# Optimization experiments

Hardware: AMD Instinct MI355X
Metric: run time of the kernel (lower is better)

## Reference

```python
import jax, jax.numpy as jnp
import numpy as np
import math

D = 512      # input_size == hidden_size
TAU = 4      # length of att/spatial lists
N = 16384    # tokens (batch*H*W)

def setup_inputs() -> dict:
    key = jax.random.key(0)
    ks = jax.random.split(key, 16)
    s = 1.0 / math.sqrt(D)
    return {
        "T_t": jax.random.normal(ks[0], (N, D), jnp.float32),
        "S_t": jax.random.normal(ks[1], (N, D), jnp.float32),
        "t_att": jax.random.normal(ks[2], (TAU, N, D), jnp.float32),
        "s_att": jax.random.normal(ks[3], (TAU, N, D), jnp.float32),
        "t_spatial": jax.random.normal(ks[4], (TAU, N, D), jnp.float32),
        "s_spatial": jax.random.normal(ks[5], (TAU, N, D), jnp.float32),
        # fl_t: Linear(D, 3D); fl_t_next: Linear(D, D); same for s
        "W_t": jax.random.uniform(ks[6], (3 * D, D), jnp.float32, -s, s),
        "b_t": jax.random.uniform(ks[7], (3 * D,), jnp.float32, -s, s),
        "W_tn": jax.random.uniform(ks[8], (D, D), jnp.float32, -s, s),
        "b_tn": jax.random.uniform(ks[9], (D,), jnp.float32, -s, s),
        "W_s": jax.random.uniform(ks[10], (3 * D, D), jnp.float32, -s, s),
        "b_s": jax.random.uniform(ks[11], (3 * D,), jnp.float32, -s, s),
        "W_sn": jax.random.uniform(ks[12], (D, D), jnp.float32, -s, s),
        "b_sn": jax.random.uniform(ks[13], (D,), jnp.float32, -s, s),
    }

def reference(T_t, S_t, t_att, s_att, t_spatial, s_spatial,
              W_t, b_t, W_tn, b_tn, W_s, b_s, W_sn, b_sn):
    d = T_t.shape[-1]
    scale = 1.0 / jnp.sqrt(jnp.asarray(d, T_t.dtype))
    s_next = S_t @ W_sn.T + b_sn          # [N, D]
    t_next = T_t @ W_tn.T + b_tn          # [N, D]

    # trend weights: dot-product along feature dim, softmax over tau axis
    w_s = jax.nn.softmax(jnp.einsum('knd,nd->kn', s_att, s_next) * scale, axis=0)
    w_t = jax.nn.softmax(jnp.einsum('knd,nd->kn', t_spatial, t_next) * scale, axis=0)
    T_trend = jnp.einsum('knd,kn->nd', t_att, w_s)      # [N, D]
    S_trend = jnp.einsum('knd,kn->nd', s_spatial, w_t)  # [N, D]

    t_gate = jax.nn.sigmoid(t_next)
    s_gate = jax.nn.sigmoid(s_next)
    T_fusion = T_t * t_gate + (1.0 - t_gate) * T_trend
    S_fusion = S_t * s_gate + (1.0 - s_gate) * S_trend

    T_concat = T_fusion @ W_t.T + b_t     # [N, 3D]
    S_concat = S_fusion @ W_s.T + b_s
    t_g, t_t, t_s = jnp.split(T_concat, 3, axis=1)
    s_g, s_t, s_s = jnp.split(S_concat, 3, axis=1)
    T_gate = jax.nn.sigmoid(t_g)
    S_gate = jax.nn.sigmoid(s_g)
    T_new = T_gate * t_t + (1.0 - T_gate) * s_t
    S_new = S_gate * s_s + (1.0 - S_gate) * t_s
    return T_new, S_new
```

## Files before the change

kernel.cpp:

```cpp
#include <hip/hip_runtime.h>

#define NTOK 16384
#define DIM 512
#define NTAU 4

typedef __attribute__((ext_vector_type(4))) float f32x4;
typedef __attribute__((ext_vector_type(8))) short bf16x8;
typedef __attribute__((ext_vector_type(4))) unsigned short u16x4;
typedef __attribute__((ext_vector_type(8))) unsigned short u16x8;

__device__ inline unsigned short f2bf(float f) {
    union { float f; unsigned int u; } v; v.f = f;
    unsigned int u = v.u + 0x7FFFu + ((v.u >> 16) & 1u);
    return (unsigned short)(u >> 16);
}

__device__ inline void bf8_to_f32(u16x8 h, f32x4& a, f32x4& b) {
    union { unsigned int u; float f; } t;
#pragma unroll
    for (int e = 0; e < 4; e++) { t.u = ((unsigned int)h[e]) << 16; a[e] = t.f; }
#pragma unroll
    for (int e = 0; e < 4; e++) { t.u = ((unsigned int)h[4 + e]) << 16; b[e] = t.f; }
}

#define NTLOAD4(p) __builtin_nontemporal_load((const f32x4*)(p))

__global__ void convert_f32_bf16(const float* __restrict__ src,
                                 unsigned short* __restrict__ dst, int n4) {
    int i = blockIdx.x * blockDim.x + threadIdx.x;
    if (i < n4) {
        f32x4 v = ((const f32x4*)src)[i];
        u16x4 o;
        o[0] = f2bf(v[0]); o[1] = f2bf(v[1]); o[2] = f2bf(v[2]); o[3] = f2bf(v[3]);
        ((u16x4*)dst)[i] = o;
    }
}

__global__ __launch_bounds__(256, 2) void gemm_next(
    const float* __restrict__ A, const unsigned short* __restrict__ W,
    const float* __restrict__ bias, unsigned short* __restrict__ out)
{
    __shared__ unsigned short lA[128][40];
    __shared__ unsigned short lB[128][40];
    const int tid = threadIdx.x;
    const int id = blockIdx.x + 4 * blockIdx.y;
    const int xcd = id & 7;
    const int idx = id >> 3;
    const int m0 = (xcd * 16 + (idx >> 2)) * 128;
    const int n0 = (idx & 3) * 128;
    const int lane = tid & 63;
    const int w = tid >> 6;
    const int wr = w >> 1, wc = w & 1;

    f32x4 acc[4][4];
#pragma unroll
    for (int i = 0; i < 4; i++)
#pragma unroll
        for (int j = 0; j < 4; j++) acc[i][j] = (f32x4){0.f, 0.f, 0.f, 0.f};

    const int arow = tid >> 3;
    const int acol = (tid & 7) * 4;
    const int brow = tid >> 2;
    const int bcol = (tid & 3) * 8;

    for (int k0 = 0; k0 < DIM; k0 += 32) {
#pragma unroll
        for (int i = 0; i < 4; i++) {
            int r = arow + 32 * i;
            f32x4 v = *(const f32x4*)(A + (size_t)(m0 + r) * DIM + k0 + acol);
            u16x4 o;
            o[0] = f2bf(v[0]); o[1] = f2bf(v[1]); o[2] = f2bf(v[2]); o[3] = f2bf(v[3]);
            *(u16x4*)&lA[r][acol] = o;
        }
#pragma unroll
        for (int i = 0; i < 2; i++) {
            int r = brow + 64 * i;
            u16x8 v = *(const u16x8*)(W + (size_t)(n0 + r) * DIM + k0 + bcol);
            *(u16x8*)&lB[r][bcol] = v;
        }
        __syncthreads();

        bf16x8 af[4], bfr[4];
#pragma unroll
        for (int i = 0; i < 4; i++)
            af[i] = *(const bf16x8*)&lA[wr * 64 + i * 16 + (lane & 15)][(lane >> 4) * 8];
#pragma unroll
        for (int j = 0; j < 4; j++)
            bfr[j] = *(const bf16x8*)&lB[wc * 64 + j * 16 + (lane & 15)][(lane >> 4) * 8];
#pragma unroll
        for (int i = 0; i < 4; i++)
#pragma unroll
            for (int j = 0; j < 4; j++)
                acc[i][j] = __builtin_amdgcn_mfma_f32_16x16x32_bf16(af[i], bfr[j], acc[i][j], 0, 0, 0);
        __syncthreads();
    }

#pragma unroll
    for (int j = 0; j < 4; j++) {
        int n = n0 + wc * 64 + j * 16 + (lane & 15);
        float bv = bias[n];
#pragma unroll
        for (int i = 0; i < 4; i++) {
            int mbase = m0 + wr * 64 + i * 16 + (lane >> 4) * 4;
#pragma unroll
            for (int r = 0; r < 4; r++)
                out[(size_t)(mbase + r) * DIM + n] = f2bf(acc[i][j][r] + bv);
        }
    }
}

__global__ __launch_bounds__(256) void fuse_stream(
    const float* __restrict__ T_t, const float* __restrict__ S_t,
    const float* __restrict__ t_att, const float* __restrict__ s_att,
    const float* __restrict__ t_spatial, const float* __restrict__ s_spatial,
    const unsigned short* __restrict__ t_next, const unsigned short* __restrict__ s_next,
    unsigned short* __restrict__ Tf, unsigned short* __restrict__ Sf)
{
    const int lane = threadIdx.x & 63;
    const int n = (blockIdx.x << 2) + (threadIdx.x >> 6);
    const int c = lane * 8;
    const size_t rb = (size_t)n * DIM + c;
    const float scale = 0.04419417382415922f;

    f32x4 tn_a, tn_b, sn_a, sn_b;
    bf8_to_f32(*(const u16x8*)(t_next + rb), tn_a, tn_b);
    bf8_to_f32(*(const u16x8*)(s_next + rb), sn_a, sn_b);

    f32x4 p1s[NTAU][2], p1t[NTAU][2];
#pragma unroll
    for (int k = 0; k < NTAU; k++) {
        const size_t kb = ((size_t)k * NTOK + n) * DIM + c;
        p1s[k][0] = NTLOAD4(s_att + kb);
        p1s[k][1] = NTLOAD4(s_att + kb + 4);
        p1t[k][0] = NTLOAD4(t_spatial + kb);
        p1t[k][1] = NTLOAD4(t_spatial + kb + 4);
    }

    float dws[NTAU], dwt[NTAU];
#pragma unroll
    for (int k = 0; k < NTAU; k++) {
        f32x4 a0 = p1s[k][0], a1 = p1s[k][1];
        f32x4 b0 = p1t[k][0], b1 = p1t[k][1];
        dws[k] = a0[0]*sn_a[0]+a0[1]*sn_a[1]+a0[2]*sn_a[2]+a0[3]*sn_a[3]
               + a1[0]*sn_b[0]+a1[1]*sn_b[1]+a1[2]*sn_b[2]+a1[3]*sn_b[3];
        dwt[k] = b0[0]*tn_a[0]+b0[1]*tn_a[1]+b0[2]*tn_a[2]+b0[3]*tn_a[3]
               + b1[0]*tn_b[0]+b1[1]*tn_b[1]+b1[2]*tn_b[2]+b1[3]*tn_b[3];
    }

    f32x4 p2t[NTAU][2], p2s[NTAU][2];
#pragma unroll
    for (int k = 0; k < NTAU; k++) {
        const size_t kb = ((size_t)k * NTOK + n) * DIM + c;
        p2t[k][0] = NTLOAD4(t_att + kb);
        p2t[k][1] = NTLOAD4(t_att + kb + 4);
        p2s[k][0] = NTLOAD4(s_spatial + kb);
        p2s[k][1] = NTLOAD4(s_spatial + kb + 4);
    }
    f32x4 Ta = *(const f32x4*)(T_t + rb);
    f32x4 Tb = *(const f32x4*)(T_t + rb + 4);
    f32x4 Sa = *(const f32x4*)(S_t + rb);
    f32x4 Sb = *(const f32x4*)(S_t + rb + 4);

#pragma unroll
    for (int k = 0; k < NTAU; k++) {
        float v = dws[k];
#pragma unroll
        for (int off = 32; off; off >>= 1) v += __shfl_xor(v, off);
        dws[k] = v * scale;
        float u = dwt[k];
#pragma unroll
        for (int off = 32; off; off >>= 1) u += __shfl_xor(u, off);
        dwt[k] = u * scale;
    }

    float ws_[NTAU], wt_[NTAU];
    {
        float ms = fmaxf(fmaxf(dws[0], dws[1]), fmaxf(dws[2], dws[3]));
        float mt = fmaxf(fmaxf(dwt[0], dwt[1]), fmaxf(dwt[2], dwt[3]));
        float ssum = 0.f, tsum = 0.f;
#pragma unroll
        for (int k = 0; k < NTAU; k++) {
            ws_[k] = __expf(dws[k] - ms); ssum += ws_[k];
            wt_[k] = __expf(dwt[k] - mt); tsum += wt_[k];
        }
        float rs = 1.f / ssum, rt = 1.f / tsum;
#pragma unroll
        for (int k = 0; k < NTAU; k++) { ws_[k] *= rs; wt_[k] *= rt; }
    }

    f32x4 Tta = {0,0,0,0}, Ttb = {0,0,0,0}, Sta = {0,0,0,0}, Stb = {0,0,0,0};
#pragma unroll
    for (int k = 0; k < NTAU; k++) {
        float wk = ws_[k], vk = wt_[k];
#pragma unroll
        for (int e = 0; e < 4; e++) {
            Tta[e] += wk * p2t[k][0][e]; Ttb[e] += wk * p2t[k][1][e];
            Sta[e] += vk * p2s[k][0][e]; Stb[e] += vk * p2s[k][1][e];
        }
    }

    u16x8 oT, oS;
#pragma unroll
    for (int e = 0; e < 4; e++) {
        float gt_a = 1.f / (1.f + __expf(-tn_a[e]));
        float gt_b = 1.f / (1.f + __expf(-tn_b[e]));
        float gs_a = 1.f / (1.f + __expf(-sn_a[e]));
        float gs_b = 1.f / (1.f + __expf(-sn_b[e]));
        oT[e]     = f2bf(Ta[e] * gt_a + (1.f - gt_a) * Tta[e]);
        oT[4 + e] = f2bf(Tb[e] * gt_b + (1.f - gt_b) * Ttb[e]);
        oS[e]     = f2bf(Sa[e] * gs_a + (1.f - gs_a) * Sta[e]);
        oS[4 + e] = f2bf(Sb[e] * gs_b + (1.f - gs_b) * Stb[e]);
    }
    *(u16x8*)(Tf + rb) = oT;
    *(u16x8*)(Sf + rb) = oS;
}

__global__ __launch_bounds__(256, 2) void gemm_final(
    const unsigned short* __restrict__ Tf, const unsigned short* __restrict__ Sf,
    const unsigned short* __restrict__ Wt, const unsigned short* __restrict__ Ws,
    const float* __restrict__ bt, const float* __restrict__ bs,
    float* __restrict__ out)
{
    __shared__ unsigned short lT[128][40];
    __shared__ unsigned short lS[128][40];
    __shared__ unsigned short lW[6][32][40];
    const int tid = threadIdx.x;
    const int id = blockIdx.x + 16 * blockIdx.y;
    const int xcd = id & 7;
    const int idx = id >> 3;
    const int m0 = (xcd * 16 + (idx >> 4)) * 128;
    const int j0 = (idx & 15) * 32;
    const int lane = tid & 63;
    const int w = tid >> 6, wr = w >> 1, wc = w & 1;

    f32x4 acc[6][4];
#pragma unroll
    for (int g = 0; g < 6; g++)
#pragma unroll
        for (int i = 0; i < 4; i++) acc[g][i] = (f32x4){0.f, 0.f, 0.f, 0.f};

    const int arow = tid >> 2;
    const int acol = (tid & 3) * 8;

    for (int k0 = 0; k0 < DIM; k0 += 32) {
#pragma unroll
        for (int i = 0; i < 2; i++) {
            int r = arow + 64 * i;
            *(u16x8*)&lT[r][acol] = *(const u16x8*)(Tf + (size_t)(m0 + r) * DIM + k0 + acol);
            *(u16x8*)&lS[r][acol] = *(const u16x8*)(Sf + (size_t)(m0 + r) * DIM + k0 + acol);
        }
#pragma unroll
        for (int i = 0; i < 3; i++) {
            int cidx = tid + 256 * i;
            int g = cidx >> 7;
            int rr = (cidx >> 2) & 31;
            int ch = (cidx & 3) * 8;
            const unsigned short* src = (g < 3) ? Wt : Ws;
            int row = (g % 3) * DIM + j0 + rr;
            *(u16x8*)&lW[g][rr][ch] = *(const u16x8*)(src + (size_t)row * DIM + k0 + ch);
        }
        __syncthreads();

        bf16x8 aT[4], aS[4];
#pragma unroll
        for (int i = 0; i < 4; i++) {
            aT[i] = *(const bf16x8*)&lT[wr * 64 + i * 16 + (lane & 15)][(lane >> 4) * 8];
            aS[i] = *(const bf16x8*)&lS[wr * 64 + i * 16 + (lane & 15)][(lane >> 4) * 8];
        }
#pragma unroll
        for (int g = 0; g < 6; g++) {
            bf16x8 bw = *(const bf16x8*)&lW[g][wc * 16 + (lane & 15)][(lane >> 4) * 8];
#pragma unroll
            for (int i = 0; i < 4; i++)
                acc[g][i] = __builtin_amdgcn_mfma_f32_16x16x32_bf16(
                    (g < 3) ? aT[i] : aS[i], bw, acc[g][i], 0, 0, 0);
        }
        __syncthreads();
    }

    const int j = j0 + wc * 16 + (lane & 15);
    const float btg = bt[j], btt = bt[512 + j], bts = bt[1024 + j];
    const float bsg = bs[j], bst = bs[512 + j], bss = bs[1024 + j];
#pragma unroll
    for (int i = 0; i < 4; i++) {
        int mbase = m0 + wr * 64 + i * 16 + (lane >> 4) * 4;
#pragma unroll
        for (int r = 0; r < 4; r++) {
            float TG = acc[0][i][r] + btg;
            float TT = acc[1][i][r] + btt;
            float TS = acc[2][i][r] + bts;
            float SG = acc[3][i][r] + bsg;
            float ST = acc[4][i][r] + bst;
            float SS = acc[5][i][r] + bss;
            float gT = 1.f / (1.f + __expf(-TG));
            float gS = 1.f / (1.f + __expf(-SG));
            size_t m = (size_t)(mbase + r);
            out[m * DIM + j] = gT * TT + (1.f - gT) * ST;
            out[(size_t)NTOK * DIM + m * DIM + j] = gS * SS + (1.f - gS) * TS;
        }
    }
}

extern "C" void kernel_launch(void* const* d_in, const int* in_sizes, int n_in,
                              void* d_out, int out_size, void* d_ws, size_t ws_size,
                              hipStream_t stream) {
    const float* T_t       = (const float*)d_in[0];
    const float* S_t       = (const float*)d_in[1];
    const float* t_att     = (const float*)d_in[2];
    const float* s_att     = (const float*)d_in[3];
    const float* t_spatial = (const float*)d_in[4];
    const float* s_spatial = (const float*)d_in[5];
    const float* W_t  = (const float*)d_in[6];
    const float* b_t  = (const float*)d_in[7];
    const float* W_tn = (const float*)d_in[8];
    const float* b_tn = (const float*)d_in[9];
    const float* W_s  = (const float*)d_in[10];
    const float* b_s  = (const float*)d_in[11];
    const float* W_sn = (const float*)d_in[12];
    const float* b_sn = (const float*)d_in[13];
    float* out = (float*)d_out;

    char* ws = (char*)d_ws;
    unsigned short* t_next = (unsigned short*)(ws + 0);
    unsigned short* s_next = (unsigned short*)(ws + 16777216);
    unsigned short* Tf     = (unsigned short*)(ws + 33554432);
    unsigned short* Sf     = (unsigned short*)(ws + 50331648);
    unsigned short* Wtn_b  = (unsigned short*)(ws + 67108864);
    unsigned short* Wsn_b  = (unsigned short*)(ws + 67633152);
    unsigned short* Wt_b   = (unsigned short*)(ws + 68157440);
    unsigned short* Ws_b   = (unsigned short*)(ws + 69730304);

    const int n_sq = 512 * 512 / 4, n_big = 1536 * 512 / 4;
    convert_f32_bf16<<<(n_sq + 255) / 256, 256, 0, stream>>>(W_tn, Wtn_b, n_sq);
    convert_f32_bf16<<<(n_sq + 255) / 256, 256, 0, stream>>>(W_sn, Wsn_b, n_sq);
    convert_f32_bf16<<<(n_big + 255) / 256, 256, 0, stream>>>(W_t, Wt_b, n_big);
    convert_f32_bf16<<<(n_big + 255) / 256, 256, 0, stream>>>(W_s, Ws_b, n_big);

    dim3 g1(DIM / 128, NTOK / 128);
    gemm_next<<<g1, 256, 0, stream>>>(T_t, Wtn_b, b_tn, t_next);
    gemm_next<<<g1, 256, 0, stream>>>(S_t, Wsn_b, b_sn, s_next);

    fuse_stream<<<4096, 256, 0, stream>>>(T_t, S_t, t_att, s_att, t_spatial, s_spatial,
                                          t_next, s_next, Tf, Sf);

    dim3 g3(DIM / 32, NTOK / 128);
    gemm_final<<<g3, 256, 0, stream>>>(Tf, Sf, Wt_b, Ws_b, b_t, b_s, out);
}
```

Baseline: 292.5 us.

## Double-buffer final GEMM with direct LDS loads, merge weight conversions, hoist stream loads

The final GEMM now double-buffers its shared-memory tiles. It fills them with global_load_lds direct-to-LDS copies using an XOR-swizzled layout instead of padded rows, so the next K tile loads while MFMAs run on the current one. The four weight-conversion launches become one kernel. In fuse_stream, all the big tau-stream loads are issued up front before any computation, so more memory traffic is in flight. The cost is higher register pressure in fuse_stream and twice the LDS footprint in the GEMM.

```diff
diff --git a/kernel.cpp b/kernel.cpp
--- a/kernel.cpp
+++ b/kernel.cpp
@@ -8,6 +8,7 @@
 typedef __attribute__((ext_vector_type(8))) short bf16x8;
 typedef __attribute__((ext_vector_type(4))) unsigned short u16x4;
 typedef __attribute__((ext_vector_type(8))) unsigned short u16x8;
+typedef unsigned int u32;
 
 __device__ inline unsigned short f2bf(float f) {
     union { float f; unsigned int u; } v; v.f = f;
@@ -25,15 +26,25 @@
 
 #define NTLOAD4(p) __builtin_nontemporal_load((const f32x4*)(p))
 
-__global__ void convert_f32_bf16(const float* __restrict__ src,
-                                 unsigned short* __restrict__ dst, int n4) {
-    int i = blockIdx.x * blockDim.x + threadIdx.x;
-    if (i < n4) {
-        f32x4 v = ((const f32x4*)src)[i];
-        u16x4 o;
-        o[0] = f2bf(v[0]); o[1] = f2bf(v[1]); o[2] = f2bf(v[2]); o[3] = f2bf(v[3]);
-        ((u16x4*)dst)[i] = o;
-    }
+__device__ __forceinline__ void gload16(const void* g, void* l) {
+    __builtin_amdgcn_global_load_lds((const __attribute__((address_space(1))) u32*)g,
+                                     (__attribute__((address_space(3))) u32*)l, 16, 0, 0);
+}
+
+__global__ void convert_all(const float* __restrict__ a, const float* __restrict__ b,
+                            const float* __restrict__ c, const float* __restrict__ d,
+                            unsigned short* __restrict__ oa, unsigned short* __restrict__ ob,
+                            unsigned short* __restrict__ oc, unsigned short* __restrict__ od) {
+    int i = blockIdx.x * 256 + threadIdx.x;
+    const float* s; unsigned short* t; int off;
+    if (i < 65536)       { s = a; t = oa; off = i; }
+    else if (i < 131072) { s = b; t = ob; off = i - 65536; }
+    else if (i < 327680) { s = c; t = oc; off = i - 131072; }
+    else                 { s = d; t = od; off = i - 327680; }
+    f32x4 v = ((const f32x4*)s)[off];
+    u16x4 o;
+    o[0] = f2bf(v[0]); o[1] = f2bf(v[1]); o[2] = f2bf(v[2]); o[3] = f2bf(v[3]);
+    ((u16x4*)t)[off] = o;
 }
 
 __global__ __launch_bounds__(256, 2) void gemm_next(
@@ -122,11 +133,9 @@
     const size_t rb = (size_t)n * DIM + c;
     const float scale = 0.04419417382415922f;
 
-    f32x4 tn_a, tn_b, sn_a, sn_b;
-    bf8_to_f32(*(const u16x8*)(t_next + rb), tn_a, tn_b);
-    bf8_to_f32(*(const u16x8*)(s_next + rb), sn_a, sn_b);
-
-    f32x4 p1s[NTAU][2], p1t[NTAU][2];
+    u16x8 hn_t = *(const u16x8*)(t_next + rb);
+    u16x8 hn_s = *(const u16x8*)(s_next + rb);
+    f32x4 p1s[NTAU][2], p1t[NTAU][2], p2t[NTAU][2], p2s[NTAU][2];
 #pragma unroll
     for (int k = 0; k < NTAU; k++) {
         const size_t kb = ((size_t)k * NTOK + n) * DIM + c;
@@ -135,6 +144,22 @@
         p1t[k][0] = NTLOAD4(t_spatial + kb);
         p1t[k][1] = NTLOAD4(t_spatial + kb + 4);
     }
+#pragma unroll
+    for (int k = 0; k < NTAU; k++) {
+        const size_t kb = ((size_t)k * NTOK + n) * DIM + c;
+        p2t[k][0] = NTLOAD4(t_att + kb);
+        p2t[k][1] = NTLOAD4(t_att + kb + 4);
+        p2s[k][0] = NTLOAD4(s_spatial + kb);
+        p2s[k][1] = NTLOAD4(s_spatial + kb + 4);
+    }
+    f32x4 Ta = *(const f32x4*)(T_t + rb);
+    f32x4 Tb = *(const f32x4*)(T_t + rb + 4);
+    f32x4 Sa = *(const f32x4*)(S_t + rb);
+    f32x4 Sb = *(const f32x4*)(S_t + rb + 4);
+
+    f32x4 tn_a, tn_b, sn_a, sn_b;
+    bf8_to_f32(hn_t, tn_a, tn_b);
+    bf8_to_f32(hn_s, sn_a, sn_b);
 
     float dws[NTAU], dwt[NTAU];
 #pragma unroll
@@ -146,21 +171,6 @@
         dwt[k] = b0[0]*tn_a[0]+b0[1]*tn_a[1]+b0[2]*tn_a[2]+b0[3]*tn_a[3]
                + b1[0]*tn_b[0]+b1[1]*tn_b[1]+b1[2]*tn_b[2]+b1[3]*tn_b[3];
     }
-
-    f32x4 p2t[NTAU][2], p2s[NTAU][2];
-#pragma unroll
-    for (int k = 0; k < NTAU; k++) {
-        const size_t kb = ((size_t)k * NTOK + n) * DIM + c;
-        p2t[k][0] = NTLOAD4(t_att + kb);
-        p2t[k][1] = NTLOAD4(t_att + kb + 4);
-        p2s[k][0] = NTLOAD4(s_spatial + kb);
-        p2s[k][1] = NTLOAD4(s_spatial + kb + 4);
-    }
-    f32x4 Ta = *(const f32x4*)(T_t + rb);
-    f32x4 Tb = *(const f32x4*)(T_t + rb + 4);
-    f32x4 Sa = *(const f32x4*)(S_t + rb);
-    f32x4 Sb = *(const f32x4*)(S_t + rb + 4);
-
 #pragma unroll
     for (int k = 0; k < NTAU; k++) {
         float v = dws[k];
@@ -221,9 +231,9 @@
     const float* __restrict__ bt, const float* __restrict__ bs,
     float* __restrict__ out)
 {
-    __shared__ unsigned short lT[128][40];
-    __shared__ unsigned short lS[128][40];
-    __shared__ unsigned short lW[6][32][40];
+    __shared__ __align__(16) unsigned short lT[2][128][32];
+    __shared__ __align__(16) unsigned short lS[2][128][32];
+    __shared__ __align__(16) unsigned short lW[2][192][32];
     const int tid = threadIdx.x;
     const int id = blockIdx.x + 16 * blockIdx.y;
     const int xcd = id & 7;
@@ -239,43 +249,61 @@
 #pragma unroll
         for (int i = 0; i < 4; i++) acc[g][i] = (f32x4){0.f, 0.f, 0.f, 0.f};
 
-    const int arow = tid >> 2;
-    const int acol = (tid & 3) * 8;
-
-    for (int k0 = 0; k0 < DIM; k0 += 32) {
-#pragma unroll
-        for (int i = 0; i < 2; i++) {
-            int r = arow + 64 * i;
-            *(u16x8*)&lT[r][acol] = *(const u16x8*)(Tf + (size_t)(m0 + r) * DIM + k0 + acol);
-            *(u16x8*)&lS[r][acol] = *(const u16x8*)(Sf + (size_t)(m0 + r) * DIM + k0 + acol);
-        }
-#pragma unroll
-        for (int i = 0; i < 3; i++) {
-            int cidx = tid + 256 * i;
-            int g = cidx >> 7;
-            int rr = (cidx >> 2) & 31;
-            int ch = (cidx & 3) * 8;
-            const unsigned short* src = (g < 3) ? Wt : Ws;
-            int row = (g % 3) * DIM + j0 + rr;
-            *(u16x8*)&lW[g][rr][ch] = *(const u16x8*)(src + (size_t)row * DIM + k0 + ch);
-        }
-        __syncthreads();
+    const int srow = lane >> 2;
+    const int sg   = lane & 3;
+
+    auto stage = [&](int buf, int kt) {
+        const int k0 = kt * 32;
+        if (w < 2) {
+            const int rbs = w * 64;
+#pragma unroll
+            for (int i = 0; i < 4; i++) {
+                const int row = rbs + i * 16 + srow;
+                const int lg = sg ^ ((row >> 1) & 3);
+                gload16(Tf + (size_t)(m0 + row) * DIM + k0 + lg * 8, &lT[buf][rbs + i * 16][0]);
+                gload16(Sf + (size_t)(m0 + row) * DIM + k0 + lg * 8, &lS[buf][rbs + i * 16][0]);
+            }
+        } else {
+            const int rbs = (w - 2) * 96;
+#pragma unroll
+            for (int i = 0; i < 6; i++) {
+                const int r = rbs + i * 16 + srow;
+                const int lg = sg ^ ((r >> 1) & 3);
+                const int g = r >> 5;
+                const unsigned short* src = (g < 3) ? Wt : Ws;
+                const int wrow = (g < 3 ? g : g - 3) * DIM + j0 + (r & 31);
+                gload16(src + (size_t)wrow * DIM + k0 + lg * 8, &lW[buf][rbs + i * 16][0]);
+            }
+        }
+    };
+
+    stage(0, 0);
+    __syncthreads();
+
+    int cur = 0;
+    for (int kt = 0; kt < 16; ++kt) {
+        if (kt < 15) stage(cur ^ 1, kt + 1);
 
         bf16x8 aT[4], aS[4];
 #pragma unroll
         for (int i = 0; i < 4; i++) {
-            aT[i] = *(const bf16x8*)&lT[wr * 64 + i * 16 + (lane & 15)][(lane >> 4) * 8];
-            aS[i] = *(const bf16x8*)&lS[wr * 64 + i * 16 + (lane & 15)][(lane >> 4) * 8];
+            const int row = wr * 64 + i * 16 + (lane & 15);
+            const int pg = (lane >> 4) ^ ((row >> 1) & 3);
+            aT[i] = *(const bf16x8*)&lT[cur][row][pg * 8];
+            aS[i] = *(const bf16x8*)&lS[cur][row][pg * 8];
         }
 #pragma unroll
         for (int g = 0; g < 6; g++) {
-            bf16x8 bw = *(const bf16x8*)&lW[g][wc * 16 + (lane & 15)][(lane >> 4) * 8];
+            const int r = g * 32 + wc * 16 + (lane & 15);
+            const int pg = (lane >> 4) ^ ((r >> 1) & 3);
+            bf16x8 bw = *(const bf16x8*)&lW[cur][r][pg * 8];
 #pragma unroll
             for (int i = 0; i < 4; i++)
                 acc[g][i] = __builtin_amdgcn_mfma_f32_16x16x32_bf16(
                     (g < 3) ? aT[i] : aS[i], bw, acc[g][i], 0, 0, 0);
         }
         __syncthreads();
+        cur ^= 1;
     }
 
     const int j = j0 + wc * 16 + (lane & 15);
@@ -330,11 +358,8 @@
     unsigned short* Wt_b   = (unsigned short*)(ws + 68157440);
     unsigned short* Ws_b   = (unsigned short*)(ws + 69730304);
 
-    const int n_sq = 512 * 512 / 4, n_big = 1536 * 512 / 4;
-    convert_f32_bf16<<<(n_sq + 255) / 256, 256, 0, stream>>>(W_tn, Wtn_b, n_sq);
-    convert_f32_bf16<<<(n_sq + 255) / 256, 256, 0, stream>>>(W_sn, Wsn_b, n_sq);
-    convert_f32_bf16<<<(n_big + 255) / 256, 256, 0, stream>>>(W_t, Wt_b, n_big);
-    convert_f32_bf16<<<(n_big + 255) / 256, 256, 0, stream>>>(W_s, Ws_b, n_big);
+    convert_all<<<2048, 256, 0, stream>>>(W_tn, W_sn, W_t, W_s,
+                                          Wtn_b, Wsn_b, Wt_b, Ws_b);
 
     dim3 g1(DIM / 128, NTOK / 128);
     gemm_next<<<g1, 256, 0, stream>>>(T_t, Wtn_b, b_tn, t_next);
```

New measurement: 288.2 us. About the same (-1.5%).
